# Optimization experiments

Measured on AMD Instinct MI355X. Metric: run time of the kernel, lower is better.

Reference implementation:

```python
import jax, jax.numpy as jnp
import numpy as np

B, S, N = 16, 64, 4096
D = 64            # input_dim*seq_len == output_dim*graph_dim
FEAT = 64
E = 32768
HEADS = (3, 3, 1)
NEG_SLOPE = 0.2   # PyG GATConv default negative_slope


def _lin_init(key, fi, fo):
    k1, k2 = jax.random.split(key)
    s = 1.0 / np.sqrt(fi)
    return (jax.random.uniform(k1, (fi, fo), jnp.float32, -s, s),
            jax.random.uniform(k2, (fo,), jnp.float32, -s, s))


def setup_inputs() -> dict:
    key = jax.random.key(0)
    ks = jax.random.split(key, 32)
    inp = {}
    inp["inputs"] = jax.random.normal(ks[0], (B, S, N, 1), jnp.float32)
    inp["edge_index"] = jax.random.randint(ks[1], (2, E), 0, N, dtype=jnp.int32)
    inp["W_seq"], inp["b_seq"] = _lin_init(ks[2], D, D)
    inp["src_embed"] = jax.random.normal(ks[3], (N, FEAT), jnp.float32) * 0.1
    inp["tgt_embed"] = jax.random.normal(ks[4], (FEAT, N), jnp.float32) * 0.1
    for i, H in enumerate(HEADS):
        s = 1.0 / np.sqrt(D)
        inp[f"Wg{i}"] = jax.random.uniform(ks[5 + 5 * i], (D, H * D), jnp.float32, -s, s)
        inp[f"asrc{i}"] = jax.random.normal(ks[6 + 5 * i], (H, D), jnp.float32) * 0.1
        inp[f"adst{i}"] = jax.random.normal(ks[7 + 5 * i], (H, D), jnp.float32) * 0.1
        inp[f"bg{i}"] = jnp.zeros((D,), jnp.float32)
        inp[f"Wl{i}"], inp[f"bl{i}"] = _lin_init(ks[8 + 5 * i], D, D)
    inp["Wo"], inp["bo"] = _lin_init(ks[25], D, D)
    return inp


def _gat(x, src, dst, W, a_src, a_dst, b):
    # PyG GATConv, concat=False (mean over heads). x: [B,N,D] -> [B,N,D]
    H, C = a_src.shape
    xp = jnp.einsum('bnd,dhc->bnhc', x, W.reshape(D, H, C))       # [B,N,H,C]
    al_s = jnp.einsum('bnhc,hc->bnh', xp, a_src)
    al_d = jnp.einsum('bnhc,hc->bnh', xp, a_dst)
    e = jax.nn.leaky_relu(al_s[:, src] + al_d[:, dst], NEG_SLOPE)  # [B,Et,H]

    def per_graph(e_b, xj_b):
        m = jax.ops.segment_max(e_b, dst, num_segments=N)          # [N,H]
        w = jnp.exp(e_b - m[dst])
        z = jax.ops.segment_sum(w, dst, num_segments=N)
        alpha = w / z[dst]                                         # softmax per dst node
        return jax.ops.segment_sum(xj_b * alpha[..., None], dst, num_segments=N)

    out = jax.vmap(per_graph)(e, xp[:, src])                       # [B,N,H,C]
    return out.mean(axis=2) + b


def _forward(inputs, edge_index, W_seq, b_seq, src_embed, tgt_embed,
             Wg0, asrc0, adst0, bg0, Wl0, bl0,
             Wg1, asrc1, adst1, bg1, Wl1, bl1,
             Wg2, asrc2, adst2, bg2, Wl2, bl2, Wo, bo):
    loop = jnp.arange(N, dtype=edge_index.dtype)
    src = jnp.concatenate([edge_index[0], loop])   # PyG add_self_loops=True
    dst = jnp.concatenate([edge_index[1], loop])
    h = inputs.transpose(0, 2, 3, 1).reshape(B * N, D)
    h = h @ W_seq + b_seq + h                       # seq_linear residual
    A = jax.nn.softmax(jax.nn.relu(src_embed @ tgt_embed), axis=1)  # learned adjacency [N,N]
    gat_p = [(Wg0, asrc0, adst0, bg0), (Wg1, asrc1, adst1, bg1), (Wg2, asrc2, adst2, bg2)]
    lin_p = [(Wl0, bl0), (Wl1, bl1), (Wl2, bl2)]
    for i in range(3):
        hb = h.reshape(B, N, D)
        # layer-0 GAT output is computed but unused in the original code (dead); skip it
        h_cur = _gat(hb, src, dst, *gat_p[i]).reshape(B * N, D) if i > 0 else None
        adp = jnp.einsum('mn,bnd->bmd', A, hb)      # adaptive-graph matmul (dropout in eval = identity)
        adp = (adp @ lin_p[i][0] + lin_p[i][1]).reshape(B * N, D)
        g = jax.nn.sigmoid(adp)
        if i == 0:
            origin = h @ Wo + bo
            h = jnp.tanh(h) * g + origin * (1.0 - g)
        elif i == 1:
            h = jax.nn.leaky_relu(h_cur, 0.01) * g + h * (1.0 - g)
        else:
            h = jax.nn.relu(h_cur) * g + h * (1.0 - g)
    return h.reshape(B, N, 1, D)   # [batch, node_num, output_dim, graph_dim]


def reference(inputs, edge_index, W_seq, b_seq, src_embed, tgt_embed,
              Wg0, asrc0, adst0, bg0, Wl0, bl0,
              Wg1, asrc1, adst1, bg1, Wl1, bl1,
              Wg2, asrc2, adst2, bg2, Wl2, bl2, Wo, bo):
    return _forward(inputs, edge_index, W_seq, b_seq, src_embed, tgt_embed,
                    Wg0, asrc0, adst0, bg0, Wl0, bl0,
                    Wg1, asrc1, adst1, bg1, Wl1, bl1,
                    Wg2, asrc2, adst2, bg2, Wl2, bl2, Wo, bo)
```

## Files before the change

### kernel.cpp

```cpp
#include <hip/hip_runtime.h>
#include <stdint.h>

#define NB 16
#define NN 4096
#define DD 64
#define EE 32768
#define ETOT 36864
#define ROWS 65536
#define KSPLIT 2

typedef _Float16 f16;
typedef f16   half8 __attribute__((ext_vector_type(8)));
typedef f16   f16x8 __attribute__((ext_vector_type(8)));
typedef f16   f16x4 __attribute__((ext_vector_type(4)));
typedef float f32x4 __attribute__((ext_vector_type(4)));

__device__ __forceinline__ void gload16(const f16* g, f16* l) {
  __builtin_amdgcn_global_load_lds((const __attribute__((address_space(1))) void*)g,
                                   (__attribute__((address_space(3))) void*)l, 16, 0, 0);
}

__global__ __launch_bounds__(256) void k_zero(int* p, int n) {
  int i = blockIdx.x * 256 + threadIdx.x;
  if (i < n) p[i] = 0;
}

__global__ __launch_bounds__(256) void k_count(const int* __restrict__ ei, int* __restrict__ cnt) {
  int t = blockIdx.x * 256 + threadIdx.x;
  if (t >= ETOT) return;
  int d = (t < EE) ? ei[EE + t] : (t - EE);
  atomicAdd(&cnt[d], 1);
}

__global__ __launch_bounds__(256) void k_scan(const int* __restrict__ cnt, int* __restrict__ offs) {
  __shared__ int part[256];
  int t = threadIdx.x;
  int loc[16]; int s = 0;
  #pragma unroll
  for (int i = 0; i < 16; ++i) { int v = cnt[(t << 4) + i]; loc[i] = s; s += v; }
  part[t] = s;
  __syncthreads();
  int own = s;
  for (int d = 1; d < 256; d <<= 1) {
    int u = (t >= d) ? part[t - d] : 0;
    __syncthreads();
    part[t] += u;
    __syncthreads();
  }
  int base = part[t] - own;
  #pragma unroll
  for (int i = 0; i < 16; ++i) offs[(t << 4) + i] = base + loc[i];
}

__global__ __launch_bounds__(256) void k_fill(const int* __restrict__ ei, const int* __restrict__ offs,
                                              int* __restrict__ cur, int* __restrict__ esrc,
                                              int* __restrict__ edst) {
  int t = blockIdx.x * 256 + threadIdx.x;
  if (t >= ETOT) return;
  int s, d;
  if (t < EE) { s = ei[t]; d = ei[EE + t]; } else { s = d = t - EE; }
  int p = atomicAdd(&cur[d], 1);
  esrc[offs[d] + p] = s;
  edst[offs[d] + p] = d;
}

__global__ __launch_bounds__(256) void k_seq(const float* __restrict__ inp, const float* __restrict__ Wseq,
                                             const float* __restrict__ bseq, float* __restrict__ h) {
  __shared__ float X[64 * 68];
  int t = threadIdx.x;
  int b = blockIdx.x >> 6, n0 = (blockIdx.x & 63) << 6;
  #pragma unroll
  for (int i = 0; i < 16; ++i) {
    int idx = t + (i << 8);
    int s = idx >> 6, nl = idx & 63;
    X[nl * 68 + s] = inp[((size_t)((b << 6) + s) << 12) + n0 + nl];
  }
  __syncthreads();
  int c = t & 63, rg = t >> 6;
  float Wc[64];
  #pragma unroll
  for (int k = 0; k < 64; ++k) Wc[k] = Wseq[(k << 6) + c];
  float bc = bseq[c];
  for (int rr = 0; rr < 16; ++rr) {
    int r = (rg << 4) + rr;
    float a = bc + X[r * 68 + c];
    #pragma unroll
    for (int k4 = 0; k4 < 16; ++k4) {
      float4 x = *(const float4*)&X[r * 68 + (k4 << 2)];
      a = fmaf(x.x, Wc[4*k4+0], a); a = fmaf(x.y, Wc[4*k4+1], a);
      a = fmaf(x.z, Wc[4*k4+2], a); a = fmaf(x.w, Wc[4*k4+3], a);
    }
    h[((size_t)(b << 12) + n0 + r) * 64 + c] = a;
  }
}

__global__ __launch_bounds__(256) void k_castSE(const float* __restrict__ SE, f16* __restrict__ SEh) {
  int i = (blockIdx.x * 256 + threadIdx.x) * 4;
  float4 v = *(const float4*)(SE + i);
  f16 o[4] = {(f16)v.x, (f16)v.y, (f16)v.z, (f16)v.w};
  *(uint64_t*)(SEh + i) = *(uint64_t*)o;
}

__global__ __launch_bounds__(256) void k_castTE(const float* __restrict__ TE, f16* __restrict__ TEh) {
  __shared__ float X[64 * 65];
  int t = threadIdx.x;
  int j0 = blockIdx.x << 6;
  #pragma unroll
  for (int i = 0; i < 16; ++i) {
    int idx = t + (i << 8);
    int k = idx >> 6, jl = idx & 63;
    X[jl * 65 + k] = TE[((size_t)k << 12) + j0 + jl];
  }
  __syncthreads();
  int jl = t >> 2, kg = t & 3;
  f16 o[16];
  #pragma unroll
  for (int i = 0; i < 16; ++i) o[i] = (f16)X[jl * 65 + (kg << 4) + i];
  f16* dst = TEh + ((size_t)(j0 + jl) << 6) + (kg << 4);
  *(uint64_t*)(dst + 0) = *(uint64_t*)(o + 0);
  *(uint64_t*)(dst + 4) = *(uint64_t*)(o + 4);
  *(uint64_t*)(dst + 8) = *(uint64_t*)(o + 8);
  *(uint64_t*)(dst + 12) = *(uint64_t*)(o + 12);
}

__global__ __launch_bounds__(256) void k_adjmm(const f16* __restrict__ SEh, const f16* __restrict__ TEh,
                                               f16* __restrict__ A, float* __restrict__ Zpart) {
  __shared__ f16 Al[128 * 32];
  __shared__ f16 Bl[128 * 32];
  const int t = threadIdx.x, lane = t & 63, w = t >> 6;
  const int m0 = blockIdx.y << 7, j0 = blockIdx.x << 7;
  const int l15 = lane & 15, lhi = lane >> 4;
  const int wm = (w >> 1) << 6, wj = (w & 1) << 6;
  f32x4 acc[4][4] = {};
  const int c0 = (w << 6) + lane;
  const int row0 = c0 >> 2, ko0 = (c0 & 3) << 3;
  const int c1 = c0 + 256;
  const int row1 = c1 >> 2, ko1 = (c1 & 3) << 3;
  const f16* ga0 = SEh + (size_t)(m0 + row0) * 64 + ko0;
  const f16* ga1 = SEh + (size_t)(m0 + row1) * 64 + ko1;
  const f16* gb0 = TEh + (size_t)(j0 + row0) * 64 + ko0;
  const f16* gb1 = TEh + (size_t)(j0 + row1) * 64 + ko1;
  f16* la0 = Al + c0 * 8; f16* la1 = Al + c1 * 8;
  f16* lb0 = Bl + c0 * 8; f16* lb1 = Bl + c1 * 8;
  for (int kt = 0; kt < 2; ++kt) {
    const int kof = kt << 5;
    gload16(ga0 + kof, la0);
    gload16(ga1 + kof, la1);
    gload16(gb0 + kof, lb0);
    gload16(gb1 + kof, lb1);
    __syncthreads();
    half8 af[4], bf[4];
    #pragma unroll
    for (int i = 0; i < 4; ++i) {
      af[i] = *(const half8*)(Al + (wm + i * 16 + l15) * 32 + lhi * 8);
      bf[i] = *(const half8*)(Bl + (wj + i * 16 + l15) * 32 + lhi * 8);
    }
    #pragma unroll
    for (int mi = 0; mi < 4; ++mi)
      #pragma unroll
      for (int nj = 0; nj < 4; ++nj)
        acc[mi][nj] = __builtin_amdgcn_mfma_f32_16x16x32_f16(af[mi], bf[nj], acc[mi][nj], 0, 0, 0);
    __syncthreads();
  }
  float rs[4][4];
  #pragma unroll
  for (int mi = 0; mi < 4; ++mi)
    #pragma unroll
    for (int r = 0; r < 4; ++r) rs[mi][r] = 0.f;
  #pragma unroll
  for (int mi = 0; mi < 4; ++mi)
    #pragma unroll
    for (int nj = 0; nj < 4; ++nj)
      #pragma unroll
      for (int r = 0; r < 4; ++r) {
        int row = m0 + wm + mi * 16 + lhi * 4 + r;
        int col = j0 + wj + nj * 16 + l15;
        float e = __expf(fmaxf(acc[mi][nj][r], 0.f));
        f16 eh = (f16)e;
        A[((size_t)row << 12) + col] = eh;
        rs[mi][r] += (float)eh;
      }
  #pragma unroll
  for (int mi = 0; mi < 4; ++mi)
    #pragma unroll
    for (int r = 0; r < 4; ++r) {
      float s = rs[mi][r];
      s += __shfl_xor(s, 1); s += __shfl_xor(s, 2);
      s += __shfl_xor(s, 4); s += __shfl_xor(s, 8);
      rs[mi][r] = s;
    }
  if (l15 == 0) {
    int p = (blockIdx.x << 1) + (w & 1);
    #pragma unroll
    for (int mi = 0; mi < 4; ++mi)
      #pragma unroll
      for (int r = 0; r < 4; ++r)
        Zpart[((size_t)p << 12) + m0 + wm + mi * 16 + lhi * 4 + r] = rs[mi][r];
  }
}

__global__ __launch_bounds__(256) void k_rowz(const float* __restrict__ Zpart, float* __restrict__ rowZ) {
  int row = blockIdx.x * 256 + threadIdx.x;
  float s = 0.f;
  #pragma unroll 8
  for (int p = 0; p < 64; ++p) s += Zpart[((size_t)p << 12) + row];
  rowZ[row] = 1.f / s;
}

#define NKT 32
__global__ __launch_bounds__(512) void k_gemm8(const f16* __restrict__ A, const f16* __restrict__ BT,
                                               f16* __restrict__ Cout) {
  extern __shared__ f16 smem[];
  const int t = threadIdx.x, lane = t & 63, wid = t >> 6;
  const int wr = wid >> 2, wc = wid & 3;
  const int l15 = lane & 15, lhi = lane >> 4;
  const int h7 = l15 & 7;
  const int wgid = blockIdx.x;
  const int nid = (wgid & 7) * 32 + (wgid >> 3);
  const int z = nid >> 7, rem = nid & 127;
  const int m0 = (rem >> 3) << 8;
  const int j0 = (rem & 7) << 7;
  const size_t kbase = (size_t)z << 11;
  f16* __restrict__ Cz = Cout + ((size_t)z << 22);

  const f16* gA[4]; int lA[4];
  #pragma unroll
  for (int i = 0; i < 4; ++i) {
    int s = t + (i << 9), row = s >> 3, sl = (s & 7) ^ (row & 7);
    gA[i] = A + (size_t)(m0 + row) * 4096 + kbase + sl * 8;
    lA[i] = s * 8;
  }
  const f16* gB[2]; int lB[2];
  #pragma unroll
  for (int i = 0; i < 2; ++i) {
    int s = t + (i << 9), row = s >> 3, sl = (s & 7) ^ (row & 7);
    gB[i] = BT + (size_t)(j0 + row) * 4096 + kbase + sl * 8;
    lB[i] = 16384 + s * 8;
  }
  #define SA(buf, kt, i) gload16(gA[i] + (kt) * 64, smem + (buf) * 24576 + lA[i])
  #define SB(buf, kt, i) gload16(gB[i] + (kt) * 64, smem + (buf) * 24576 + lB[i])

  const int rbase = wr << 7;
  const int cbase = wc << 5;
  f32x4 acc[8][2] = {};

  #pragma unroll
  for (int i = 0; i < 4; ++i) SA(0, 0, i);
  #pragma unroll
  for (int i = 0; i < 2; ++i) SB(0, 0, i);
  #pragma unroll
  for (int i = 0; i < 4; ++i) SA(1, 1, i);
  #pragma unroll
  for (int i = 0; i < 2; ++i) SB(1, 1, i);
  asm volatile("s_waitcnt vmcnt(6)" ::: "memory");
  __builtin_amdgcn_sched_barrier(0);
  __builtin_amdgcn_s_barrier();
  __builtin_amdgcn_sched_barrier(0);

  int b0 = 0, b1 = 1, b2 = 2;
  for (int kt = 0; kt < NKT; ++kt) {
    const f16* Ab = smem + b0 * 24576;
    const f16* Bb = Ab + 16384;
    const bool pf = (kt + 2 < NKT);
    {
      half8 af[8], bf[2];
      #pragma unroll
      for (int mi = 0; mi < 8; ++mi) {
        int row = rbase + mi * 16 + l15;
        af[mi] = *(const half8*)(Ab + row * 64 + (lhi ^ h7) * 8);
      }
      #pragma unroll
      for (int nj = 0; nj < 2; ++nj) {
        int row = cbase + nj * 16 + l15;
        bf[nj] = *(const half8*)(Bb + row * 64 + (lhi ^ h7) * 8);
      }
      if (pf) { SA(b2, kt + 2, 0); SA(b2, kt + 2, 1); SA(b2, kt + 2, 2); }
      __builtin_amdgcn_s_setprio(1);
      #pragma unroll
      for (int mi = 0; mi < 8; ++mi)
        #pragma unroll
        for (int nj = 0; nj < 2; ++nj)
          acc[mi][nj] = __builtin_amdgcn_mfma_f32_16x16x32_f16(af[mi], bf[nj], acc[mi][nj], 0, 0, 0);
      __builtin_amdgcn_s_setprio(0);
    }
    __builtin_amdgcn_s_barrier();
    __builtin_amdgcn_sched_barrier(0);
    {
      half8 af[8], bf[2];
      #pragma unroll
      for (int mi = 0; mi < 8; ++mi) {
        int row = rbase + mi * 16 + l15;
        af[mi] = *(const half8*)(Ab + row * 64 + ((4 + lhi) ^ h7) * 8);
      }
      #pragma unroll
      for (int nj = 0; nj < 2; ++nj) {
        int row = cbase + nj * 16 + l15;
        bf[nj] = *(const half8*)(Bb + row * 64 + ((4 + lhi) ^ h7) * 8);
      }
      if (pf) { SA(b2, kt + 2, 3); SB(b2, kt + 2, 0); SB(b2, kt + 2, 1); }
      __builtin_amdgcn_s_setprio(1);
      #pragma unroll
      for (int mi = 0; mi < 8; ++mi)
        #pragma unroll
        for (int nj = 0; nj < 2; ++nj)
          acc[mi][nj] = __builtin_amdgcn_mfma_f32_16x16x32_f16(af[mi], bf[nj], acc[mi][nj], 0, 0, 0);
      __builtin_amdgcn_s_setprio(0);
    }
    if (kt < NKT - 2)       asm volatile("s_waitcnt vmcnt(6)" ::: "memory");
    else if (kt == NKT - 2) asm volatile("s_waitcnt vmcnt(0)" ::: "memory");
    __builtin_amdgcn_sched_barrier(0);
    __builtin_amdgcn_s_barrier();
    __builtin_amdgcn_sched_barrier(0);
    int tb = b0; b0 = b1; b1 = b2; b2 = tb;
  }
  #undef SA
  #undef SB
  #pragma unroll
  for (int mi = 0; mi < 8; ++mi)
    #pragma unroll
    for (int nj = 0; nj < 2; ++nj)
      #pragma unroll
      for (int r = 0; r < 4; ++r) {
        int row = m0 + rbase + mi * 16 + (lhi << 2) + r;
        int col = j0 + cbase + nj * 16 + l15;
        Cz[(size_t)row * 1024 + col] = (f16)acc[mi][nj][r];
      }
}

template<int H, int NP>
__global__ __launch_bounds__(256) void k_wprep(const float* __restrict__ Wg, const float* __restrict__ asrc,
                                               const float* __restrict__ adst, const float* __restrict__ Wl,
                                               f16* __restrict__ Wgh) {
  const int WL0 = H * 64 + 16;
  for (int i = blockIdx.x * 256 + threadIdx.x; i < NP * 64; i += 16 * 256) {
    int j = i >> 6, k = i & 63;
    float v;
    if (j < H * 64) {
      v = Wg[(size_t)k * (H * 64) + j];
    } else if (j < H * 64 + 2 * H) {
      int cc = j - H * 64, hh = cc >> 1;
      const float* a = ((cc & 1) ? adst : asrc) + (hh << 6);
      const float* wrow = Wg + (size_t)k * (H * 64) + (hh << 6);
      float s = 0.f;
      #pragma unroll 16
      for (int c = 0; c < 64; ++c) s = fmaf(wrow[c], a[c], s);
      v = s;
    } else if (j >= WL0 && j < WL0 + 64) {
      v = Wl[(k << 6) + (j - WL0)];
    } else v = 0.f;
    Wgh[(size_t)j * 64 + k] = (f16)v;
  }
}

__global__ __launch_bounds__(256) void k_w0prep(const float* __restrict__ Wl0, const float* __restrict__ Wo,
                                                f16* __restrict__ W0h) {
  for (int i = blockIdx.x * 256 + threadIdx.x; i < 128 * 64; i += 8 * 256) {
    int j = i >> 6, k = i & 63;
    float v = (j < 64) ? Wl0[(k << 6) + j] : Wo[(k << 6) + (j - 64)];
    W0h[(size_t)j * 64 + k] = (f16)v;
  }
}

template<int H, int NP>
__global__ __launch_bounds__(256) void k_xpmm(const float* __restrict__ h, const f16* __restrict__ Wgh,
                                              f16* __restrict__ xp, float* __restrict__ als,
                                              float* __restrict__ ald, f16* __restrict__ HWlT) {
  const int WL0 = H * 64 + 16, JW0 = WL0 / 16, NT = NP / 16;
  __shared__ f16 Ah[64 * 72];
  __shared__ f16 Bh[NP * 72];
  __shared__ f16 stage[64 * 72];
  const int t = threadIdx.x, lane = t & 63, w = t >> 6;
  const size_t r0 = (size_t)blockIdx.x * 64;
  const int b = (int)(r0 >> 12), n0 = (int)(r0 & 4095);
  #pragma unroll
  for (int i = 0; i < 4; ++i) {
    int idx = t + (i << 8);
    int row = idx >> 4, k4 = (idx & 15) << 2;
    float4 v = *(const float4*)&h[(r0 + row) * 64 + k4];
    f16 o[4] = {(f16)v.x, (f16)v.y, (f16)v.z, (f16)v.w};
    *(uint64_t*)&Ah[row * 72 + k4] = *(uint64_t*)o;
  }
  for (int i = t; i < NP * 16; i += 256) {
    int row = i >> 4, k4 = (i & 15) << 2;
    *(uint64_t*)&Bh[row * 72 + k4] = *(const uint64_t*)&Wgh[(size_t)row * 64 + k4];
  }
  __syncthreads();
  const int l15 = lane & 15, lhi = lane >> 4;
  f32x4 acc[NT] = {};
  #pragma unroll
  for (int kk = 0; kk < 2; ++kk) {
    half8 af = *(const half8*)&Ah[(w * 16 + l15) * 72 + kk * 32 + lhi * 8];
    #pragma unroll
    for (int j = 0; j < NT; ++j) {
      half8 bf = *(const half8*)&Bh[(j * 16 + l15) * 72 + kk * 32 + lhi * 8];
      acc[j] = __builtin_amdgcn_mfma_f32_16x16x32_f16(af, bf, acc[j], 0, 0, 0);
    }
  }
  const int rl = w * 16 + lhi * 4;
  #pragma unroll
  for (int j = 0; j < NT; ++j) {
    int col = j * 16 + l15;
    if (j * 16 + 15 < H * 64) {
      #pragma unroll
      for (int r = 0; r < 4; ++r)
        xp[(r0 + rl + r) * (H * 64) + col] = (f16)acc[j][r];
    } else if (j < JW0) {
      int cc = col - H * 64;
      if (cc >= 0 && cc < 2 * H) {
        int hh = cc >> 1;
        #pragma unroll
        for (int r = 0; r < 4; ++r) {
          if (cc & 1) ald[(r0 + rl + r) * H + hh] = acc[j][r];
          else        als[(r0 + rl + r) * H + hh] = acc[j][r];
        }
      }
    } else {
      int e = col - WL0;
      f16 o[4] = {(f16)acc[j][0], (f16)acc[j][1], (f16)acc[j][2], (f16)acc[j][3]};
      *(uint64_t*)&stage[e * 72 + rl] = *(uint64_t*)o;
    }
  }
  __syncthreads();
  {
    int e = t >> 2, seg = (t & 3) << 4;
    float4 v0 = *(const float4*)&stage[e * 72 + seg];
    float4 v1 = *(const float4*)&stage[e * 72 + seg + 8];
    f16* dst = HWlT + (((size_t)((b << 6) + e)) << 12) + n0 + seg;
    *(float4*)dst = v0;
    *(float4*)(dst + 8) = v1;
  }
}

__global__ __launch_bounds__(256) void k_prep0(const float* __restrict__ h, const f16* __restrict__ W0h,
                                               f16* __restrict__ HWlT, f16* __restrict__ orig) {
  __shared__ f16 Ah[64 * 72];
  __shared__ f16 Bh[128 * 72];
  __shared__ f16 stage[64 * 72];
  const int t = threadIdx.x, lane = t & 63, w = t >> 6;
  const size_t r0 = (size_t)blockIdx.x * 64;
  const int b = (int)(r0 >> 12), n0 = (int)(r0 & 4095);
  #pragma unroll
  for (int i = 0; i < 4; ++i) {
    int idx = t + (i << 8);
    int row = idx >> 4, k4 = (idx & 15) << 2;
    float4 v = *(const float4*)&h[(r0 + row) * 64 + k4];
    f16 o[4] = {(f16)v.x, (f16)v.y, (f16)v.z, (f16)v.w};
    *(uint64_t*)&Ah[row * 72 + k4] = *(uint64_t*)o;
  }
  for (int i = t; i < 128 * 16; i += 256) {
    int row = i >> 4, k4 = (i & 15) << 2;
    *(uint64_t*)&Bh[row * 72 + k4] = *(const uint64_t*)&W0h[(size_t)row * 64 + k4];
  }
  __syncthreads();
  const int l15 = lane & 15, lhi = lane >> 4;
  f32x4 acc[8] = {};
  #pragma unroll
  for (int kk = 0; kk < 2; ++kk) {
    half8 af = *(const half8*)&Ah[(w * 16 + l15) * 72 + kk * 32 + lhi * 8];
    #pragma unroll
    for (int j = 0; j < 8; ++j) {
      half8 bf = *(const half8*)&Bh[(j * 16 + l15) * 72 + kk * 32 + lhi * 8];
      acc[j] = __builtin_amdgcn_mfma_f32_16x16x32_f16(af, bf, acc[j], 0, 0, 0);
    }
  }
  const int rl = w * 16 + lhi * 4;
  #pragma unroll
  for (int j = 0; j < 8; ++j) {
    int col = j * 16 + l15;
    if (j < 4) {
      f16 o[4] = {(f16)acc[j][0], (f16)acc[j][1], (f16)acc[j][2], (f16)acc[j][3]};
      *(uint64_t*)&stage[col * 72 + rl] = *(uint64_t*)o;
    } else {
      #pragma unroll
      for (int r = 0; r < 4; ++r)
        orig[(r0 + rl + r) * 64 + (col - 64)] = (f16)acc[j][r];
    }
  }
  __syncthreads();
  {
    int e = t >> 2, seg = (t & 3) << 4;
    float4 v0 = *(const float4*)&stage[e * 72 + seg];
    float4 v1 = *(const float4*)&stage[e * 72 + seg + 8];
    f16* dst = HWlT + (((size_t)((b << 6) + e)) << 12) + n0 + seg;
    *(float4*)dst = v0;
    *(float4*)(dst + 8) = v1;
  }
}

template<int H>
__global__ __launch_bounds__(256) void k_maxals(const float* __restrict__ als, float* __restrict__ Mals) {
  __shared__ float red[256];
  int b = blockIdx.x, t = threadIdx.x;
  size_t rbase = (size_t)b << 12;
  for (int h = 0; h < H; ++h) {
    float m = -1e30f;
    for (int n = t; n < NN; n += 256) m = fmaxf(m, als[(rbase + n) * H + h]);
    red[t] = m;
    __syncthreads();
    for (int d = 128; d; d >>= 1) {
      if (t < d) red[t] = fmaxf(red[t], red[t + d]);
      __syncthreads();
    }
    if (t == 0) Mals[b * H + h] = red[0];
    __syncthreads();
  }
}

template<int H>
__global__ __launch_bounds__(256) void k_wts(const float* __restrict__ als, const float* __restrict__ ald,
                                             const float* __restrict__ Mals, const int* __restrict__ esrc,
                                             const int* __restrict__ edst, float* __restrict__ wts) {
  int t = threadIdx.x, lane = t & 63, w = t >> 6;
  int gw = blockIdx.x * 4 + w;
  int b = gw & 15;
  int p = ((gw >> 4) << 6) + lane;
  size_t rbase = (size_t)b << 12;
  int s = esrc[p], n = edst[p];
  float* dst = wts + ((size_t)b * ETOT + p) * H;
  #pragma unroll
  for (int h = 0; h < H; ++h) {
    float ad = ald[(rbase + n) * H + h];
    float B = Mals[b * H + h] + ad;
    float T = B > 0.f ? B : 0.2f * B;
    float ev = als[(rbase + s) * H + h] + ad;
    ev = ev > 0.f ? ev : 0.2f * ev;
    dst[h] = __expf(ev - T);
  }
}

template<int H>
__global__ __launch_bounds__(256) void k_agg(const f16* __restrict__ xp, const float* __restrict__ wts,
                                             const int* __restrict__ offs, const int* __restrict__ cnt,
                                             const int* __restrict__ esrc, const float* __restrict__ bg,
                                             float* __restrict__ hcur) {
  __shared__ float wbuf[4][H * 64];
  __shared__ int   sbuf[4][64];
  int t = threadIdx.x, lane = t & 63, wv = t >> 6;
  int wid = (blockIdx.x << 2) + wv;
  int b = wid >> 12, n = wid & 4095;
  size_t rbase = (size_t)b << 12;
  int o = offs[n], c = cnt[n];
  const float* wsrc = wts + ((size_t)b * ETOT + o) * H;
  float z[H], acc[H];
  #pragma unroll
  for (int hh = 0; hh < H; ++hh) { z[hh] = 0.f; acc[hh] = 0.f; }
  for (int e0 = 0; e0 < c; e0 += 64) {
    int ce = min(64, c - e0);
    if (lane < ce) {
      sbuf[wv][lane] = esrc[o + e0 + lane];
      #pragma unroll
      for (int hh = 0; hh < H; ++hh)
        wbuf[wv][hh * 64 + lane] = wsrc[(size_t)(e0 + lane) * H + hh];
    }
    for (int e = 0; e < ce; ++e) {
      int s = sbuf[wv][e];
      const f16* row = xp + (rbase + s) * (size_t)(H * 64) + lane;
      #pragma unroll
      for (int hh = 0; hh < H; ++hh) {
        float wv_ = wbuf[wv][hh * 64 + e];
        z[hh] += wv_;
        acc[hh] = fmaf(wv_, (float)row[hh << 6], acc[hh]);
      }
    }
  }
  float r = 0.f;
  #pragma unroll
  for (int hh = 0; hh < H; ++hh) r += acc[hh] / z[hh];
  hcur[(rbase + n) * 64 + lane] = r * (1.f / H) + bg[lane];
}

__global__ __launch_bounds__(256) void k_comb0e(const float* __restrict__ h, const f16* __restrict__ gp,
                                                const float* __restrict__ rowZ, const f16* __restrict__ orig,
                                                const float* __restrict__ bl, const float* __restrict__ bo,
                                                float* __restrict__ hout) {
  for (size_t i4 = (size_t)blockIdx.x * 256 + threadIdx.x; i4 < (size_t)ROWS * 16; i4 += (size_t)2048 * 256) {
    size_t i = i4 * 4;
    int d = (int)(i & 63), n = (int)((i >> 6) & 4095), b = (int)(i >> 18);
    size_t ga = ((size_t)n << 10) + (b << 6) + d;
    float zi = rowZ[n];
    f16x4 g0 = *(const f16x4*)&gp[ga];
    f16x4 g1 = *(const f16x4*)&gp[ga + (size_t)(4096 * 1024)];
    f16x4 og = *(const f16x4*)&orig[i];
    float4 hv = *(const float4*)&h[i];
    float4 o;
    float* op = &o.x;
    const float* hp = &hv.x;
    #pragma unroll
    for (int r = 0; r < 4; ++r) {
      float g = 1.f / (1.f + __expf(-(((float)g0[r] + (float)g1[r]) * zi + bl[d + r])));
      float orv = (float)og[r] + bo[d + r];
      op[r] = tanhf(hp[r]) * g + orv * (1.f - g);
    }
    *(float4*)&hout[i] = o;
  }
}

template<int ACT>
__global__ __launch_bounds__(256) void k_comb12e(const float* __restrict__ h, const f16* __restrict__ gp,
                                                 const float* __restrict__ rowZ, const float* __restrict__ hcur,
                                                 const float* __restrict__ bl, float* __restrict__ hout) {
  for (size_t i4 = (size_t)blockIdx.x * 256 + threadIdx.x; i4 < (size_t)ROWS * 16; i4 += (size_t)2048 * 256) {
    size_t i = i4 * 4;
    int d = (int)(i & 63), n = (int)((i >> 6) & 4095), b = (int)(i >> 18);
    size_t ga = ((size_t)n << 10) + (b << 6) + d;
    float zi = rowZ[n];
    f16x4 g0 = *(const f16x4*)&gp[ga];
    f16x4 g1 = *(const f16x4*)&gp[ga + (size_t)(4096 * 1024)];
    float4 hv = *(const float4*)&h[i];
    float4 cv = *(const float4*)&hcur[i];
    float4 o;
    float* op = &o.x;
    const float* hp = &hv.x;
    const float* cp = &cv.x;
    #pragma unroll
    for (int r = 0; r < 4; ++r) {
      float g = 1.f / (1.f + __expf(-(((float)g0[r] + (float)g1[r]) * zi + bl[d + r])));
      float act = ACT ? fmaxf(cp[r], 0.f) : (cp[r] > 0.f ? cp[r] : 0.01f * cp[r]);
      op[r] = act * g + hp[r] * (1.f - g);
    }
    *(float4*)&hout[i] = o;
  }
}

extern "C" void kernel_launch(void* const* d_in, const int* in_sizes, int n_in,
                              void* d_out, int out_size, void* d_ws, size_t ws_size,
                              hipStream_t stream) {
  (void)in_sizes; (void)n_in; (void)out_size; (void)ws_size;
  const float* inp  = (const float*)d_in[0];
  const int*   ei   = (const int*)d_in[1];
  const float* Wseq = (const float*)d_in[2];
  const float* bseq = (const float*)d_in[3];
  const float* SE   = (const float*)d_in[4];
  const float* TE   = (const float*)d_in[5];
  const float* Wg[3]   = {(const float*)d_in[6],  (const float*)d_in[12], (const float*)d_in[18]};
  const float* asrc[3] = {(const float*)d_in[7],  (const float*)d_in[13], (const float*)d_in[19]};
  const float* adst[3] = {(const float*)d_in[8],  (const float*)d_in[14], (const float*)d_in[20]};
  const float* bgp[3]  = {(const float*)d_in[9],  (const float*)d_in[15], (const float*)d_in[21]};
  const float* Wl[3]   = {(const float*)d_in[10], (const float*)d_in[16], (const float*)d_in[22]};
  const float* bl[3]   = {(const float*)d_in[11], (const float*)d_in[17], (const float*)d_in[23]};
  const float* Wo = (const float*)d_in[24];
  const float* bo = (const float*)d_in[25];
  float* out = (float*)d_out;

  uint8_t* ws = (uint8_t*)d_ws;
  size_t o = 0;
  auto nxt = [&](size_t sz) { void* p = ws + o; o += (sz + 255) & ~(size_t)255; return p; };
  f16*   Af   = (f16*)  nxt((size_t)NN * NN * sizeof(f16));
  f16*   HWlT = (f16*)  nxt((size_t)1024 * NN * sizeof(f16));
  float* h    = (float*)nxt((size_t)ROWS * 64 * 4);
  f16*   gp   = (f16*)  nxt((size_t)KSPLIT * NN * 1024 * sizeof(f16));
  f16*   xp   = (f16*)  nxt((size_t)ROWS * 192 * sizeof(f16));
  f16*   orig = (f16*)  nxt((size_t)ROWS * 64 * sizeof(f16));
  float* als  = (float*)nxt((size_t)ROWS * 3 * 4);
  float* ald  = (float*)nxt((size_t)ROWS * 3 * 4);
  float* hcur = (float*)nxt((size_t)ROWS * 64 * 4);
  float* rowZ = (float*)nxt((size_t)NN * 4);
  float* Zpart= (float*)nxt((size_t)64 * NN * 4);
  f16*   SEh  = (f16*)  nxt((size_t)NN * 64 * sizeof(f16));
  f16*   TEh  = (f16*)  nxt((size_t)NN * 64 * sizeof(f16));
  f16*   Wgh  = (f16*)  nxt((size_t)288 * 64 * sizeof(f16));
  f16*   W0h  = (f16*)  nxt((size_t)128 * 64 * sizeof(f16));
  float* wts  = (float*)nxt((size_t)NB * ETOT * 3 * 4);
  float* Mals = (float*)nxt((size_t)NB * 3 * 4);
  int*   cnt  = (int*)  nxt((size_t)NN * 4);
  int*   curp = (int*)  nxt((size_t)NN * 4);
  int*   offs = (int*)  nxt((size_t)NN * 4);
  int*   esrc = (int*)  nxt((size_t)ETOT * 4);
  int*   edst = (int*)  nxt((size_t)ETOT * 4);

  static bool attr_set = false;
  if (!attr_set) {
    hipFuncSetAttribute((const void*)k_gemm8, hipFuncAttributeMaxDynamicSharedMemorySize, 147456);
    attr_set = true;
  }

  dim3 blk(256);
  k_zero<<<16, blk, 0, stream>>>(cnt, NN);
  k_zero<<<16, blk, 0, stream>>>(curp, NN);
  k_count<<<144, blk, 0, stream>>>(ei, cnt);
  k_scan<<<1, blk, 0, stream>>>(cnt, offs);
  k_fill<<<144, blk, 0, stream>>>(ei, offs, curp, esrc, edst);
  k_seq<<<1024, blk, 0, stream>>>(inp, Wseq, bseq, h);
  k_castSE<<<256, blk, 0, stream>>>(SE, SEh);
  k_castTE<<<64, blk, 0, stream>>>(TE, TEh);
  k_adjmm<<<dim3(32, 32), blk, 0, stream>>>(SEh, TEh, Af, Zpart);
  k_rowz<<<16, blk, 0, stream>>>(Zpart, rowZ);
  k_w0prep<<<8, blk, 0, stream>>>(Wl[0], Wo, W0h);
  k_prep0<<<1024, blk, 0, stream>>>(h, W0h, HWlT, orig);
  k_gemm8<<<256, 512, 147456, stream>>>(Af, HWlT, gp);
  k_comb0e<<<2048, blk, 0, stream>>>(h, gp, rowZ, orig, bl[0], bo, h);
  k_wprep<3, 272><<<16, blk, 0, stream>>>(Wg[1], asrc[1], adst[1], Wl[1], Wgh);
  k_xpmm<3, 272><<<1024, blk, 0, stream>>>(h, Wgh, xp, als, ald, HWlT);
  k_maxals<3><<<16, blk, 0, stream>>>(als, Mals);
  k_wts<3><<<2304, blk, 0, stream>>>(als, ald, Mals, esrc, edst, wts);
  k_gemm8<<<256, 512, 147456, stream>>>(Af, HWlT, gp);
  k_agg<3><<<16384, blk, 0, stream>>>(xp, wts, offs, cnt, esrc, bgp[1], hcur);
  k_comb12e<0><<<2048, blk, 0, stream>>>(h, gp, rowZ, hcur, bl[1], h);
  k_wprep<1, 144><<<16, blk, 0, stream>>>(Wg[2], asrc[2], adst[2], Wl[2], Wgh);
  k_xpmm<1, 144><<<1024, blk, 0, stream>>>(h, Wgh, xp, als, ald, HWlT);
  k_maxals<1><<<16, blk, 0, stream>>>(als, Mals);
  k_wts<1><<<2304, blk, 0, stream>>>(als, ald, Mals, esrc, edst, wts);
  k_gemm8<<<256, 512, 147456, stream>>>(Af, HWlT, gp);
  k_agg<1><<<16384, blk, 0, stream>>>(xp, wts, offs, cnt, esrc, bgp[2], hcur);
  k_comb12e<1><<<2048, blk, 0, stream>>>(h, gp, rowZ, hcur, bl[2], out);
}
```

Measured before the change: 331.8 us.

## Interleave GAT head features and weights, merge prep kernels, single-sync adjacency loads

Stores the 3-head projected features interleaved per channel (stride 4) and pads the per-edge attention weights to float4, so the aggregation kernel does one vector load per edge instead of three strided scalar loads. Merges the zeroing, cast and weight-prep kernels into fewer launches. The adjacency matmul now loads both K tiles into double-sized LDS behind one barrier. The cost is larger xp and wts buffers (padding) and more LDS in the adjacency kernel.

Result: no change. 328.4 us (-1.0%).

```diff
diff --git a/kernel.cpp b/kernel.cpp
--- a/kernel.cpp
+++ b/kernel.cpp
@@ -20,9 +20,10 @@
                                    (__attribute__((address_space(3))) void*)l, 16, 0, 0);
 }
 
-__global__ __launch_bounds__(256) void k_zero(int* p, int n) {
+__global__ __launch_bounds__(256) void k_zero2(int* a, int* b) {
   int i = blockIdx.x * 256 + threadIdx.x;
-  if (i < n) p[i] = 0;
+  if (i < NN) a[i] = 0;
+  else if (i < 2 * NN) b[i - NN] = 0;
 }
 
 __global__ __launch_bounds__(256) void k_count(const int* __restrict__ ei, int* __restrict__ cnt) {
@@ -94,17 +95,18 @@
   }
 }
 
-__global__ __launch_bounds__(256) void k_castSE(const float* __restrict__ SE, f16* __restrict__ SEh) {
-  int i = (blockIdx.x * 256 + threadIdx.x) * 4;
-  float4 v = *(const float4*)(SE + i);
-  f16 o[4] = {(f16)v.x, (f16)v.y, (f16)v.z, (f16)v.w};
-  *(uint64_t*)(SEh + i) = *(uint64_t*)o;
-}
-
-__global__ __launch_bounds__(256) void k_castTE(const float* __restrict__ TE, f16* __restrict__ TEh) {
+__global__ __launch_bounds__(256) void k_cast(const float* __restrict__ SE, const float* __restrict__ TE,
+                                              f16* __restrict__ SEh, f16* __restrict__ TEh) {
   __shared__ float X[64 * 65];
   int t = threadIdx.x;
-  int j0 = blockIdx.x << 6;
+  if (blockIdx.x < 256) {
+    int i = (blockIdx.x * 256 + t) * 4;
+    float4 v = *(const float4*)(SE + i);
+    f16 o[4] = {(f16)v.x, (f16)v.y, (f16)v.z, (f16)v.w};
+    *(uint64_t*)(SEh + i) = *(uint64_t*)o;
+    return;
+  }
+  int j0 = (blockIdx.x - 256) << 6;
   #pragma unroll
   for (int i = 0; i < 16; ++i) {
     int idx = t + (i << 8);
@@ -125,8 +127,8 @@
 
 __global__ __launch_bounds__(256) void k_adjmm(const f16* __restrict__ SEh, const f16* __restrict__ TEh,
                                                f16* __restrict__ A, float* __restrict__ Zpart) {
-  __shared__ f16 Al[128 * 32];
-  __shared__ f16 Bl[128 * 32];
+  __shared__ f16 Al[2][128 * 32];
+  __shared__ f16 Bl[2][128 * 32];
   const int t = threadIdx.x, lane = t & 63, w = t >> 6;
   const int m0 = blockIdx.y << 7, j0 = blockIdx.x << 7;
   const int l15 = lane & 15, lhi = lane >> 4;
@@ -140,27 +142,28 @@
   const f16* ga1 = SEh + (size_t)(m0 + row1) * 64 + ko1;
   const f16* gb0 = TEh + (size_t)(j0 + row0) * 64 + ko0;
   const f16* gb1 = TEh + (size_t)(j0 + row1) * 64 + ko1;
-  f16* la0 = Al + c0 * 8; f16* la1 = Al + c1 * 8;
-  f16* lb0 = Bl + c0 * 8; f16* lb1 = Bl + c1 * 8;
+  #pragma unroll
   for (int kt = 0; kt < 2; ++kt) {
     const int kof = kt << 5;
-    gload16(ga0 + kof, la0);
-    gload16(ga1 + kof, la1);
-    gload16(gb0 + kof, lb0);
-    gload16(gb1 + kof, lb1);
-    __syncthreads();
+    gload16(ga0 + kof, Al[kt] + c0 * 8);
+    gload16(ga1 + kof, Al[kt] + c1 * 8);
+    gload16(gb0 + kof, Bl[kt] + c0 * 8);
+    gload16(gb1 + kof, Bl[kt] + c1 * 8);
+  }
+  __syncthreads();
+  #pragma unroll
+  for (int kt = 0; kt < 2; ++kt) {
     half8 af[4], bf[4];
     #pragma unroll
     for (int i = 0; i < 4; ++i) {
-      af[i] = *(const half8*)(Al + (wm + i * 16 + l15) * 32 + lhi * 8);
-      bf[i] = *(const half8*)(Bl + (wj + i * 16 + l15) * 32 + lhi * 8);
+      af[i] = *(const half8*)(Al[kt] + (wm + i * 16 + l15) * 32 + lhi * 8);
+      bf[i] = *(const half8*)(Bl[kt] + (wj + i * 16 + l15) * 32 + lhi * 8);
     }
     #pragma unroll
     for (int mi = 0; mi < 4; ++mi)
       #pragma unroll
       for (int nj = 0; nj < 4; ++nj)
         acc[mi][nj] = __builtin_amdgcn_mfma_f32_16x16x32_f16(af[mi], bf[nj], acc[mi][nj], 0, 0, 0);
-    __syncthreads();
   }
   float rs[4][4];
   #pragma unroll
@@ -328,11 +331,11 @@
 }
 
 template<int H, int NP>
-__global__ __launch_bounds__(256) void k_wprep(const float* __restrict__ Wg, const float* __restrict__ asrc,
-                                               const float* __restrict__ adst, const float* __restrict__ Wl,
-                                               f16* __restrict__ Wgh) {
+__device__ __forceinline__ void wprep_body(const float* __restrict__ Wg, const float* __restrict__ asrc,
+                                           const float* __restrict__ adst, const float* __restrict__ Wl,
+                                           f16* __restrict__ Wgh, int bid, int t) {
   const int WL0 = H * 64 + 16;
-  for (int i = blockIdx.x * 256 + threadIdx.x; i < NP * 64; i += 16 * 256) {
+  for (int i = bid * 256 + t; i < NP * 64; i += 16 * 256) {
     int j = i >> 6, k = i & 63;
     float v;
     if (j < H * 64) {
@@ -352,12 +355,21 @@
   }
 }
 
-__global__ __launch_bounds__(256) void k_w0prep(const float* __restrict__ Wl0, const float* __restrict__ Wo,
-                                                f16* __restrict__ W0h) {
-  for (int i = blockIdx.x * 256 + threadIdx.x; i < 128 * 64; i += 8 * 256) {
-    int j = i >> 6, k = i & 63;
-    float v = (j < 64) ? Wl0[(k << 6) + j] : Wo[(k << 6) + (j - 64)];
-    W0h[(size_t)j * 64 + k] = (f16)v;
+__global__ __launch_bounds__(256) void k_allprep(
+    const float* __restrict__ Wg1, const float* __restrict__ as1, const float* __restrict__ ad1,
+    const float* __restrict__ Wl1, f16* __restrict__ Wgh1,
+    const float* __restrict__ Wg2, const float* __restrict__ as2, const float* __restrict__ ad2,
+    const float* __restrict__ Wl2, f16* __restrict__ Wgh2,
+    const float* __restrict__ Wl0, const float* __restrict__ Wo, f16* __restrict__ W0h) {
+  int bid = blockIdx.x, t = threadIdx.x;
+  if (bid < 16) wprep_body<3, 272>(Wg1, as1, ad1, Wl1, Wgh1, bid, t);
+  else if (bid < 32) wprep_body<1, 144>(Wg2, as2, ad2, Wl2, Wgh2, bid - 16, t);
+  else {
+    for (int i = (bid - 32) * 256 + t; i < 128 * 64; i += 8 * 256) {
+      int j = i >> 6, k = i & 63;
+      float v = (j < 64) ? Wl0[(k << 6) + j] : Wo[(k << 6) + (j - 64)];
+      W0h[(size_t)j * 64 + k] = (f16)v;
+    }
   }
 }
 
@@ -402,8 +414,10 @@
     int col = j * 16 + l15;
     if (j * 16 + 15 < H * 64) {
       #pragma unroll
-      for (int r = 0; r < 4; ++r)
-        xp[(r0 + rl + r) * (H * 64) + col] = (f16)acc[j][r];
+      for (int r = 0; r < 4; ++r) {
+        if (H == 3) xp[(r0 + rl + r) * 256 + ((col & 63) << 2) + (col >> 6)] = (f16)acc[j][r];
+        else        xp[(r0 + rl + r) * 64 + col] = (f16)acc[j][r];
+      }
     } else if (j < JW0) {
       int cc = col - H * 64;
       if (cc >= 0 && cc < 2 * H) {
@@ -510,13 +524,14 @@
 __global__ __launch_bounds__(256) void k_wts(const float* __restrict__ als, const float* __restrict__ ald,
                                              const float* __restrict__ Mals, const int* __restrict__ esrc,
                                              const int* __restrict__ edst, float* __restrict__ wts) {
+  const int WST = (H == 3) ? 4 : 1;
   int t = threadIdx.x, lane = t & 63, w = t >> 6;
   int gw = blockIdx.x * 4 + w;
   int b = gw & 15;
   int p = ((gw >> 4) << 6) + lane;
   size_t rbase = (size_t)b << 12;
   int s = esrc[p], n = edst[p];
-  float* dst = wts + ((size_t)b * ETOT + p) * H;
+  float* dst = wts + ((size_t)b * ETOT + p) * WST;
   #pragma unroll
   for (int h = 0; h < H; ++h) {
     float ad = ald[(rbase + n) * H + h];
@@ -533,14 +548,15 @@
                                              const int* __restrict__ offs, const int* __restrict__ cnt,
                                              const int* __restrict__ esrc, const float* __restrict__ bg,
                                              float* __restrict__ hcur) {
-  __shared__ float wbuf[4][H * 64];
+  const int WST = (H == 3) ? 4 : 1;
+  __shared__ float wbuf[4][64 * WST];
   __shared__ int   sbuf[4][64];
   int t = threadIdx.x, lane = t & 63, wv = t >> 6;
   int wid = (blockIdx.x << 2) + wv;
   int b = wid >> 12, n = wid & 4095;
   size_t rbase = (size_t)b << 12;
   int o = offs[n], c = cnt[n];
-  const float* wsrc = wts + ((size_t)b * ETOT + o) * H;
+  const float* wsrc = wts + ((size_t)b * ETOT + o) * WST;
   float z[H], acc[H];
   #pragma unroll
   for (int hh = 0; hh < H; ++hh) { z[hh] = 0.f; acc[hh] = 0.f; }
@@ -548,18 +564,22 @@
     int ce = min(64, c - e0);
     if (lane < ce) {
       sbuf[wv][lane] = esrc[o + e0 + lane];
-      #pragma unroll
-      for (int hh = 0; hh < H; ++hh)
-        wbuf[wv][hh * 64 + lane] = wsrc[(size_t)(e0 + lane) * H + hh];
-    }
+      if (H == 3) *(float4*)&wbuf[wv][lane * 4] = *(const float4*)&wsrc[(size_t)(e0 + lane) * 4];
+      else        wbuf[wv][lane] = wsrc[e0 + lane];
+    }
+    #pragma unroll 4
     for (int e = 0; e < ce; ++e) {
       int s = sbuf[wv][e];
-      const f16* row = xp + (rbase + s) * (size_t)(H * 64) + lane;
-      #pragma unroll
-      for (int hh = 0; hh < H; ++hh) {
-        float wv_ = wbuf[wv][hh * 64 + e];
-        z[hh] += wv_;
-        acc[hh] = fmaf(wv_, (float)row[hh << 6], acc[hh]);
+      if (H == 3) {
+        float4 w4 = *(const float4*)&wbuf[wv][e * 4];
+        f16x4 q = *(const f16x4*)(xp + (((size_t)(rbase + s)) << 8) + (lane << 2));
+        z[0] += w4.x; acc[0] = fmaf(w4.x, (float)q[0], acc[0]);
+        z[1] += w4.y; acc[1] = fmaf(w4.y, (float)q[1], acc[1]);
+        z[2] += w4.z; acc[2] = fmaf(w4.z, (float)q[2], acc[2]);
+      } else {
+        float wv_ = wbuf[wv][e];
+        float xv = (float)xp[(((size_t)(rbase + s)) << 6) + lane];
+        z[0] += wv_; acc[0] = fmaf(wv_, xv, acc[0]);
       }
     }
   }
@@ -649,7 +669,7 @@
   f16*   HWlT = (f16*)  nxt((size_t)1024 * NN * sizeof(f16));
   float* h    = (float*)nxt((size_t)ROWS * 64 * 4);
   f16*   gp   = (f16*)  nxt((size_t)KSPLIT * NN * 1024 * sizeof(f16));
-  f16*   xp   = (f16*)  nxt((size_t)ROWS * 192 * sizeof(f16));
+  f16*   xp   = (f16*)  nxt((size_t)ROWS * 256 * sizeof(f16));
   f16*   orig = (f16*)  nxt((size_t)ROWS * 64 * sizeof(f16));
   float* als  = (float*)nxt((size_t)ROWS * 3 * 4);
   float* ald  = (float*)nxt((size_t)ROWS * 3 * 4);
@@ -658,9 +678,10 @@
   float* Zpart= (float*)nxt((size_t)64 * NN * 4);
   f16*   SEh  = (f16*)  nxt((size_t)NN * 64 * sizeof(f16));
   f16*   TEh  = (f16*)  nxt((size_t)NN * 64 * sizeof(f16));
-  f16*   Wgh  = (f16*)  nxt((size_t)288 * 64 * sizeof(f16));
+  f16*   Wgh1 = (f16*)  nxt((size_t)288 * 64 * sizeof(f16));
+  f16*   Wgh2 = (f16*)  nxt((size_t)144 * 64 * sizeof(f16));
   f16*   W0h  = (f16*)  nxt((size_t)128 * 64 * sizeof(f16));
-  float* wts  = (float*)nxt((size_t)NB * ETOT * 3 * 4);
+  float* wts  = (float*)nxt((size_t)NB * ETOT * 4 * 4);
   float* Mals = (float*)nxt((size_t)NB * 3 * 4);
   int*   cnt  = (int*)  nxt((size_t)NN * 4);
   int*   curp = (int*)  nxt((size_t)NN * 4);
@@ -675,29 +696,27 @@
   }
 
   dim3 blk(256);
-  k_zero<<<16, blk, 0, stream>>>(cnt, NN);
-  k_zero<<<16, blk, 0, stream>>>(curp, NN);
+  k_zero2<<<32, blk, 0, stream>>>(cnt, curp);
   k_count<<<144, blk, 0, stream>>>(ei, cnt);
   k_scan<<<1, blk, 0, stream>>>(cnt, offs);
   k_fill<<<144, blk, 0, stream>>>(ei, offs, curp, esrc, edst);
+  k_allprep<<<40, blk, 0, stream>>>(Wg[1], asrc[1], adst[1], Wl[1], Wgh1,
+                                    Wg[2], asrc[2], adst[2], Wl[2], Wgh2,
+                                    Wl[0], Wo, W0h);
   k_seq<<<1024, blk, 0, stream>>>(inp, Wseq, bseq, h);
-  k_castSE<<<256, blk, 0, stream>>>(SE, SEh);
-  k_castTE<<<64, blk, 0, stream>>>(TE, TEh);
+  k_cast<<<320, blk, 0, stream>>>(SE, TE, SEh, TEh);
   k_adjmm<<<dim3(32, 32), blk, 0, stream>>>(SEh, TEh, Af, Zpart);
   k_rowz<<<16, blk, 0, stream>>>(Zpart, rowZ);
-  k_w0prep<<<8, blk, 0, stream>>>(Wl[0], Wo, W0h);
   k_prep0<<<1024, blk, 0, stream>>>(h, W0h, HWlT, orig);
   k_gemm8<<<256, 512, 147456, stream>>>(Af, HWlT, gp);
   k_comb0e<<<2048, blk, 0, stream>>>(h, gp, rowZ, orig, bl[0], bo, h);
-  k_wprep<3, 272><<<16, blk, 0, stream>>>(Wg[1], asrc[1], adst[1], Wl[1], Wgh);
-  k_xpmm<3, 272><<<1024, blk, 0, stream>>>(h, Wgh, xp, als, ald, HWlT);
+  k_xpmm<3, 272><<<1024, blk, 0, stream>>>(h, Wgh1, xp, als, ald, HWlT);
   k_maxals<3><<<16, blk, 0, stream>>>(als, Mals);
   k_wts<3><<<2304, blk, 0, stream>>>(als, ald, Mals, esrc, edst, wts);
   k_gemm8<<<256, 512, 147456, stream>>>(Af, HWlT, gp);
   k_agg<3><<<16384, blk, 0, stream>>>(xp, wts, offs, cnt, esrc, bgp[1], hcur);
   k_comb12e<0><<<2048, blk, 0, stream>>>(h, gp, rowZ, hcur, bl[1], h);
-  k_wprep<1, 144><<<16, blk, 0, stream>>>(Wg[2], asrc[2], adst[2], Wl[2], Wgh);
-  k_xpmm<1, 144><<<1024, blk, 0, stream>>>(h, Wgh, xp, als, ald, HWlT);
+  k_xpmm<1, 144><<<1024, blk, 0, stream>>>(h, Wgh2, xp, als, ald, HWlT);
   k_maxals<1><<<16, blk, 0, stream>>>(als, Mals);
   k_wts<1><<<2304, blk, 0, stream>>>(als, ald, Mals, esrc, edst, wts);
   k_gemm8<<<256, 512, 147456, stream>>>(Af, HWlT, gp);
```
